# Performance work log

Hardware: AMD Instinct MI355X
Metric: run time of the kernel (lower is better)

Reference implementation:

```python
import jax, jax.numpy as jnp
import numpy as np

D_MODEL = 1024
D_STATE = 16
D_CONV = 4
D_INNER = 2 * D_MODEL  # expand=2
DT_RANK = D_MODEL // D_STATE  # ceil(1024/16) = 64


def setup_inputs() -> dict:
    key = jax.random.key(0)
    ks = jax.random.split(key, 8)
    rn = lambda k, shape, s: jax.random.normal(k, shape, jnp.float32) * s
    return {
        "x": jax.random.normal(ks[0], (4, 50, 10240), jnp.float32),
        "in_proj_w": rn(ks[1], (2 * D_INNER, D_MODEL), 0.02),
        "conv_w": rn(ks[2], (D_INNER, D_CONV), 0.2),
        "conv_b": jnp.zeros((D_INNER,), jnp.float32),
        "x_proj_w": rn(ks[3], (DT_RANK + 2 * D_STATE, D_INNER), 0.02),
        "dt_proj_w": rn(ks[4], (D_INNER, DT_RANK), 0.1),
        "dt_proj_b": jnp.log(jnp.expm1(jnp.full((D_INNER,), 0.01, jnp.float32))),
        "A_log": jnp.log(jnp.tile(jnp.arange(1, D_STATE + 1, dtype=jnp.float32), (D_INNER, 1))),
        "D": jnp.ones((D_INNER,), jnp.float32),
        "out_proj_w": rn(ks[5], (D_MODEL, D_INNER), 0.02),
        "fc1_w": rn(ks[6], (D_MODEL, 10240), 0.01),
        "fc1_b": jnp.zeros((D_MODEL,), jnp.float32),
    }


def _mamba(x, in_proj_w, conv_w, conv_b, x_proj_w, dt_proj_w, dt_proj_b, A_log, Dp, out_proj_w):
    # x: (B, L, d_model)
    B, L, _ = x.shape
    xz = x @ in_proj_w.T                          # (B, L, 2*d_inner)
    xi, z = jnp.split(xz, 2, axis=-1)             # (B, L, d_inner) each
    # causal depthwise conv1d along L
    xc = jnp.transpose(xi, (0, 2, 1))             # (B, d_inner, L)
    kern = conv_w[:, None, :]                     # (d_inner, 1, K)
    xc = jax.lax.conv_general_dilated(
        xc, kern, window_strides=(1,), padding=[(D_CONV - 1, 0)],
        dimension_numbers=("NCH", "OIH", "NCH"), feature_group_count=D_INNER)
    xc = jax.nn.silu(jnp.transpose(xc, (0, 2, 1)) + conv_b)  # (B, L, d_inner)
    # input-dependent SSM parameters
    x_dbl = xc @ x_proj_w.T                       # (B, L, dt_rank + 2*N)
    dt, Bm, Cm = jnp.split(x_dbl, [DT_RANK, DT_RANK + D_STATE], axis=-1)
    delta = jax.nn.softplus(dt @ dt_proj_w.T + dt_proj_b)    # (B, L, d_inner)
    A = -jnp.exp(A_log)                           # (d_inner, N)
    dA = jnp.exp(delta[..., None] * A)            # (B, L, d_inner, N)
    dBu = delta[..., None] * Bm[:, :, None, :] * xc[..., None]

    def step(h, ab):
        a, b = ab
        h = a * h + b
        return h, h

    h0 = jnp.zeros((B, D_INNER, D_STATE), x.dtype)
    hs = jax.lax.scan(step, h0, (jnp.swapaxes(dA, 0, 1), jnp.swapaxes(dBu, 0, 1)))[1]  # (L, B, d_inner, N)
    y = jnp.einsum("lbdn,bln->bld", hs, Cm) + xc * Dp       # (B, L, d_inner)
    y = y * jax.nn.silu(z)
    return y @ out_proj_w.T                       # (B, L, d_model)


def reference(x, in_proj_w, conv_w, conv_b, x_proj_w, dt_proj_w, dt_proj_b, A_log, D, out_proj_w, fc1_w, fc1_b):
    b, c, l = x.shape
    xm = x.reshape(b, c * 10, l // 10)            # (b, c*10, 1024)
    xm = _mamba(xm, in_proj_w, conv_w, conv_b, x_proj_w, dt_proj_w, dt_proj_b, A_log, D, out_proj_w)
    xm = xm.reshape(b, c, l)                      # (b, c, 10240)
    # dropout is identity in eval mode
    return jnp.tanh(xm @ fc1_w.T + fc1_b)         # (b, c, 1024)
```

## Files before the change

kernel.cpp:

```cpp
#include <hip/hip_runtime.h>
#include <math.h>

#define BDIM 256

constexpr int B_  = 4;
constexpr int L_  = 500;
constexpr int DM  = 1024;
constexpr int DI  = 2048;
constexpr int DXZ = 4096;
constexpr int RNK = 64;
constexpr int NST = 16;
constexpr int NXP = 96;
constexpr int M1  = B_ * L_;
constexpr int M2  = 200;
constexpr int K2  = 10240;
constexpr int NC  = 20;
constexpr int LC  = L_ / NC;

typedef __attribute__((ext_vector_type(8))) __bf16 bf16x8;
typedef __attribute__((ext_vector_type(4))) __bf16 bf16x4;
typedef __attribute__((ext_vector_type(4))) float  f32x4;

__device__ __forceinline__ float sigmoidf_(float x) { return 1.0f / (1.0f + __expf(-x)); }

template<int TR>
__device__ __forceinline__ void load_tile(const float* __restrict__ G, int ldg, int valid,
                                          float4* rg, int tid)
{
    #pragma unroll
    for (int i = 0; i < TR / 32; ++i) {
        int f = tid + i * 256;
        int r = f >> 3;
        int c = (f & 7) << 2;
        float4 v = make_float4(0.f, 0.f, 0.f, 0.f);
        if (r < valid) v = *(const float4*)(G + (size_t)r * ldg + c);
        rg[i] = v;
    }
}

template<int TR>
__device__ __forceinline__ void write_tile(const float4* rg, __bf16 (*H)[40], __bf16 (*Lo)[40], int tid)
{
    #pragma unroll
    for (int i = 0; i < TR / 32; ++i) {
        int f = tid + i * 256;
        int r = f >> 3;
        int c = (f & 7) << 2;
        float vv[4] = {rg[i].x, rg[i].y, rg[i].z, rg[i].w};
        bf16x4 hv, lv;
        #pragma unroll
        for (int j = 0; j < 4; ++j) {
            __bf16 h = (__bf16)vv[j];
            hv[j] = h;
            lv[j] = (__bf16)(vv[j] - (float)h);
        }
        *(bf16x4*)&H[r][c]  = hv;
        *(bf16x4*)&Lo[r][c] = lv;
    }
}

template<int BM, int BN, int FM, int FN, int FUSE>
__global__ __launch_bounds__(256)
void gemm_mfma(const float* __restrict__ A, int lda,
               const float* __restrict__ Bw, int ldb,
               float* __restrict__ C, int ldc,
               int M, int N, int Kchunk, long csplit_stride,
               const float* __restrict__ bias)
{
    __shared__ __bf16 Ah[BM][40], Al[BM][40], Bh[BN][40], Bl[BN][40];
    const int tid  = threadIdx.x;
    const int lane = tid & 63;
    const int wave = tid >> 6;
    const int wm = wave >> 1, wn = wave & 1;
    const int m0 = blockIdx.y * BM;
    const int n0 = blockIdx.x * BN;
    const long kbase = (long)blockIdx.z * Kchunk;
    const float* Ap = A + (size_t)m0 * lda + kbase;
    const float* Bp = Bw + (size_t)n0 * ldb + kbase;
    const int validA = min(BM, M - m0);
    const int validB = min(BN, N - n0);
    f32x4 acc[FM][FN] = {};
    const int fr = lane & 15;
    const int kq = (lane >> 4) * 8;

    float4 ra[BM / 32], rb[BN / 32];
    load_tile<BM>(Ap, lda, validA, ra, tid);
    load_tile<BN>(Bp, ldb, validB, rb, tid);

    for (int k0 = 0; k0 < Kchunk; k0 += 32) {
        write_tile<BM>(ra, Ah, Al, tid);
        write_tile<BN>(rb, Bh, Bl, tid);
        __syncthreads();
        if (k0 + 32 < Kchunk) {
            load_tile<BM>(Ap + k0 + 32, lda, validA, ra, tid);
            load_tile<BN>(Bp + k0 + 32, ldb, validB, rb, tid);
        }
        bf16x8 ah[FM], al[FM], bh[FN], bl[FN];
        #pragma unroll
        for (int i = 0; i < FM; ++i) {
            int r = wm * (FM * 16) + i * 16 + fr;
            ah[i] = *(const bf16x8*)&Ah[r][kq];
            al[i] = *(const bf16x8*)&Al[r][kq];
        }
        #pragma unroll
        for (int j = 0; j < FN; ++j) {
            int r = wn * (FN * 16) + j * 16 + fr;
            bh[j] = *(const bf16x8*)&Bh[r][kq];
            bl[j] = *(const bf16x8*)&Bl[r][kq];
        }
        #pragma unroll
        for (int i = 0; i < FM; ++i)
            #pragma unroll
            for (int j = 0; j < FN; ++j) {
                acc[i][j] = __builtin_amdgcn_mfma_f32_16x16x32_bf16(ah[i], bh[j], acc[i][j], 0, 0, 0);
                acc[i][j] = __builtin_amdgcn_mfma_f32_16x16x32_bf16(ah[i], bl[j], acc[i][j], 0, 0, 0);
                acc[i][j] = __builtin_amdgcn_mfma_f32_16x16x32_bf16(al[i], bh[j], acc[i][j], 0, 0, 0);
            }
        __syncthreads();
    }

    float* Cp = C + (size_t)blockIdx.z * csplit_stride;
    #pragma unroll
    for (int i = 0; i < FM; ++i)
        #pragma unroll
        for (int j = 0; j < FN; ++j)
            #pragma unroll
            for (int r = 0; r < 4; ++r) {
                int gm = m0 + wm * (FM * 16) + i * 16 + (lane >> 4) * 4 + r;
                int gn = n0 + wn * (FN * 16) + j * 16 + (lane & 15);
                if (gm < M && gn < N) {
                    float v = acc[i][j][r];
                    if (FUSE == 1) { v += bias[gn]; v = (v > 20.f) ? v : log1pf(__expf(v)); }
                    Cp[(size_t)gm * ldc + gn] = v;
                }
            }
}

template<int FUSE>
__global__ __launch_bounds__(256)
void reduce_k(const float* __restrict__ part, float* __restrict__ C,
              int MN, int N, int S, long stride, const float* __restrict__ bias)
{
    int i = blockIdx.x * 256 + threadIdx.x;
    if (i >= MN) return;
    float s = 0.f;
    for (int j = 0; j < S; ++j) s += part[(size_t)j * stride + i];
    if (FUSE == 2) s = tanhf(s + bias[i % N]);
    C[i] = s;
}

__global__ __launch_bounds__(BDIM)
void conv_silu_k(const float* __restrict__ xz, const float* __restrict__ cw,
                 const float* __restrict__ cb, float* __restrict__ xc)
{
    int idx = blockIdx.x * BDIM + threadIdx.x;
    if (idx >= M1 * DI) return;
    int d = idx & (DI - 1);
    int m = idx >> 11;
    int b = m / L_, l = m - b * L_;
    float acc = cb[d];
    #pragma unroll
    for (int t = 0; t < 4; ++t) {
        int ls = l - 3 + t;
        if (ls >= 0)
            acc = fmaf(cw[d * 4 + t], xz[(size_t)(b * L_ + ls) * DXZ + d], acc);
    }
    xc[idx] = acc * sigmoidf_(acc);
}


__global__ __launch_bounds__(BDIM)
void scan_partial_k(const float* __restrict__ delta, const float* __restrict__ xc,
                    const float* __restrict__ xdbl, const float* __restrict__ A_log,
                    float* __restrict__ hpart, float* __restrict__ aprod)
{
    const int t = blockIdx.x * BDIM + threadIdx.x;
    const int d = t & (DI - 1);
    const int bc = t >> 11;
    const int b = bc / NC, c = bc - b * NC;
    const int l0 = c * LC;
    float Aa[NST];
    #pragma unroll
    for (int q = 0; q < 4; ++q) {
        float4 a4 = *(const float4*)(A_log + (size_t)d * NST + q * 4);
        Aa[q*4+0] = -__expf(a4.x); Aa[q*4+1] = -__expf(a4.y);
        Aa[q*4+2] = -__expf(a4.z); Aa[q*4+3] = -__expf(a4.w);
    }
    const float* dlt = delta + ((size_t)(b * L_ + l0)) * DI + d;
    const float* xcd = xc    + ((size_t)(b * L_ + l0)) * DI + d;
    const float* bp  = xdbl  + ((size_t)(b * L_ + l0)) * NXP + RNK;
    float h[NST] = {};
    float sdv = 0.f;
    for (int l = 0; l < LC; ++l) {
        float dv = dlt[(size_t)l * DI];
        float xv = xcd[(size_t)l * DI];
        const float4* b4 = (const float4*)(bp + (size_t)l * NXP);
        float dvx = dv * xv;
        sdv += dv;
        #pragma unroll
        for (int q = 0; q < 4; ++q) {
            float4 Bq = b4[q];
            float bb[4] = {Bq.x, Bq.y, Bq.z, Bq.w};
            #pragma unroll
            for (int j = 0; j < 4; ++j) {
                int n = q * 4 + j;
                float dA = __expf(dv * Aa[n]);
                h[n] = fmaf(dA, h[n], dvx * bb[j]);
            }
        }
    }
    float4* hp4 = (float4*)(hpart + (size_t)t * NST);
    float4* ap4 = (float4*)(aprod + (size_t)t * NST);
    #pragma unroll
    for (int q = 0; q < 4; ++q) {
        hp4[q] = make_float4(h[q*4], h[q*4+1], h[q*4+2], h[q*4+3]);
        ap4[q] = make_float4(__expf(Aa[q*4+0]*sdv), __expf(Aa[q*4+1]*sdv),
                             __expf(Aa[q*4+2]*sdv), __expf(Aa[q*4+3]*sdv));
    }
}

__global__ __launch_bounds__(BDIM)
void scan_fix_k(float* __restrict__ hpart, const float* __restrict__ aprod)
{
    const int i = blockIdx.x * BDIM + threadIdx.x;
    if (i >= B_ * DI * NST) return;
    const int nn = i & (NST - 1);
    const int d  = (i >> 4) & (DI - 1);
    const int b  = i >> 15;
    float h = 0.f;
    for (int c = 0; c < NC; ++c) {
        size_t o = ((size_t)((b * NC + c) * DI + d)) * NST + nn;
        float hp = hpart[o];
        float ap = aprod[o];
        hpart[o] = h;
        h = fmaf(ap, h, hp);
    }
}

__global__ __launch_bounds__(BDIM)
void scan_final_k(const float* __restrict__ xz, const float* __restrict__ xc,
                  const float* __restrict__ xdbl, const float* __restrict__ delta,
                  const float* __restrict__ A_log, const float* __restrict__ Dp,
                  const float* __restrict__ hpre, float* __restrict__ y)
{
    const int t = blockIdx.x * BDIM + threadIdx.x;
    const int d = t & (DI - 1);
    const int bc = t >> 11;
    const int b = bc / NC, c = bc - b * NC;
    const int l0 = c * LC;
    float Aa[NST];
    #pragma unroll
    for (int q = 0; q < 4; ++q) {
        float4 a4 = *(const float4*)(A_log + (size_t)d * NST + q * 4);
        Aa[q*4+0] = -__expf(a4.x); Aa[q*4+1] = -__expf(a4.y);
        Aa[q*4+2] = -__expf(a4.z); Aa[q*4+3] = -__expf(a4.w);
    }
    float h[NST];
    const float4* h4 = (const float4*)(hpre + (size_t)t * NST);
    #pragma unroll
    for (int q = 0; q < 4; ++q) {
        float4 hv = h4[q];
        h[q*4+0] = hv.x; h[q*4+1] = hv.y; h[q*4+2] = hv.z; h[q*4+3] = hv.w;
    }
    const float Dd = Dp[d];
    const float* dlt = delta + ((size_t)(b * L_ + l0)) * DI + d;
    const float* xcd = xc    + ((size_t)(b * L_ + l0)) * DI + d;
    const float* bp  = xdbl  + ((size_t)(b * L_ + l0)) * NXP + RNK;
    const float* zp  = xz    + ((size_t)(b * L_ + l0)) * DXZ + DI + d;
    float* yp = y + ((size_t)(b * L_ + l0)) * DI + d;
    for (int l = 0; l < LC; ++l) {
        float dv = dlt[(size_t)l * DI];
        float xv = xcd[(size_t)l * DI];
        const float4* b4 = (const float4*)(bp + (size_t)l * NXP);
        float dvx = dv * xv;
        float p = 0.f;
        #pragma unroll
        for (int q = 0; q < 4; ++q) {
            float4 Bq = b4[q];
            float4 Cq = b4[4 + q];
            float bb[4] = {Bq.x, Bq.y, Bq.z, Bq.w};
            float cc[4] = {Cq.x, Cq.y, Cq.z, Cq.w};
            #pragma unroll
            for (int j = 0; j < 4; ++j) {
                int n = q * 4 + j;
                float dA = __expf(dv * Aa[n]);
                h[n] = fmaf(dA, h[n], dvx * bb[j]);
                p = fmaf(h[n], cc[j], p);
            }
        }
        float zv = zp[(size_t)l * DXZ];
        float yv = fmaf(xv, Dd, p);
        yv *= zv * sigmoidf_(zv);
        yp[(size_t)l * DI] = yv;
    }
}

extern "C" void kernel_launch(void* const* d_in, const int* in_sizes, int n_in,
                              void* d_out, int out_size, void* d_ws, size_t ws_size,
                              hipStream_t stream) {
    const float* x         = (const float*)d_in[0];
    const float* in_proj_w = (const float*)d_in[1];
    const float* conv_w    = (const float*)d_in[2];
    const float* conv_b    = (const float*)d_in[3];
    const float* x_proj_w  = (const float*)d_in[4];
    const float* dt_proj_w = (const float*)d_in[5];
    const float* dt_proj_b = (const float*)d_in[6];
    const float* A_log     = (const float*)d_in[7];
    const float* Dp        = (const float*)d_in[8];
    const float* out_proj_w= (const float*)d_in[9];
    const float* fc1_w     = (const float*)d_in[10];
    const float* fc1_b     = (const float*)d_in[11];
    float* out = (float*)d_out;

    float* ws    = (float*)d_ws;
    float* xz    = ws;
    float* xc    = xz + (size_t)M1 * DXZ;
    float* xdbl  = xc + (size_t)M1 * DI;
    float* delta = xdbl + (size_t)M1 * NXP;
    float* hpart = delta + (size_t)M1 * DI;
    float* aprod = hpart + (size_t)B_ * NC * DI * NST;
    float* y     = delta;
    float* partx = delta;
    float* partO = xz;
    float* ym    = xc;
    float* partf = delta;

    dim3 blk(BDIM);
    gemm_mfma<64,128,2,4,0><<<dim3(DXZ/128, (M1+63)/64, 1), blk, 0, stream>>>(
        x, DM, in_proj_w, DM, xz, DXZ, M1, DXZ, DM, 0, nullptr);
    conv_silu_k<<<(M1*DI + BDIM-1)/BDIM, blk, 0, stream>>>(xz, conv_w, conv_b, xc);
    gemm_mfma<64,64,2,2,0><<<dim3((NXP+63)/64, (M1+63)/64, 8), blk, 0, stream>>>(
        xc, DI, x_proj_w, DI, partx, NXP, M1, NXP, DI/8, (long)M1*NXP, nullptr);
    reduce_k<0><<<(M1*NXP + 255)/256, blk, 0, stream>>>(
        partx, xdbl, M1*NXP, NXP, 8, (long)M1*NXP, nullptr);
    gemm_mfma<64,64,2,2,1><<<dim3(DI/64, (M1+63)/64, 1), blk, 0, stream>>>(
        xdbl, NXP, dt_proj_w, RNK, delta, DI, M1, DI, RNK, 0, dt_proj_b);
    scan_partial_k<<<(B_*NC*DI)/BDIM, blk, 0, stream>>>(
        delta, xc, xdbl, A_log, hpart, aprod);
    scan_fix_k<<<(B_*DI*NST + BDIM-1)/BDIM, blk, 0, stream>>>(hpart, aprod);
    scan_final_k<<<(B_*NC*DI)/BDIM, blk, 0, stream>>>(
        xz, xc, xdbl, delta, A_log, Dp, hpart, y);
    gemm_mfma<64,64,2,2,0><<<dim3(DM/64, (M1+63)/64, 4), blk, 0, stream>>>(
        y, DI, out_proj_w, DI, partO, DM, M1, DM, DI/4, (long)M1*DM, nullptr);
    reduce_k<0><<<(M1*DM + 255)/256, blk, 0, stream>>>(
        partO, ym, M1*DM, DM, 4, (long)M1*DM, nullptr);
    gemm_mfma<64,64,2,2,0><<<dim3(DM/64, (M2+63)/64, 20), blk, 0, stream>>>(
        ym, K2, fc1_w, K2, partf, DM, M2, DM, K2/20, (long)M2*DM, nullptr);
    reduce_k<2><<<(M2*DM + 255)/256, blk, 0, stream>>>(
        partf, out, M2*DM, DM, 20, (long)M2*DM, fc1_b);
    (void)in_sizes; (void)n_in; (void)out_size; (void)ws_size;
}
```

Baseline: 288.7 us.

## Pre-split weights into bf16 hi/lo once per GEMM and enlarge in_proj tile

Adds a split kernel that converts each fp32 weight matrix into bf16 high and low halves in workspace before its GEMM. The GEMM then loads the pre-split weights directly instead of converting them per tile in every block, which removes repeated conversion work and halves the weight load width. The in_proj GEMM also moves to 128x128 tiles. The cost is extra split-kernel launches and memory passes each call, plus careful reuse of workspace regions that alias live buffers.

Measured after the change: 288.9 us. No clear change (+0.1%).

```diff
diff --git a/kernel.cpp b/kernel.cpp
--- a/kernel.cpp
+++ b/kernel.cpp
@@ -23,6 +23,25 @@
 
 __device__ __forceinline__ float sigmoidf_(float x) { return 1.0f / (1.0f + __expf(-x)); }
 
+__global__ __launch_bounds__(BDIM)
+void split_w_k(const float* __restrict__ W, __bf16* __restrict__ Wh,
+               __bf16* __restrict__ Wl, int n4)
+{
+    int i = blockIdx.x * BDIM + threadIdx.x;
+    if (i >= n4) return;
+    float4 v = *(const float4*)(W + (size_t)i * 4);
+    float vv[4] = {v.x, v.y, v.z, v.w};
+    bf16x4 hv, lv;
+    #pragma unroll
+    for (int j = 0; j < 4; ++j) {
+        __bf16 h = (__bf16)vv[j];
+        hv[j] = h;
+        lv[j] = (__bf16)(vv[j] - (float)h);
+    }
+    *(bf16x4*)(Wh + (size_t)i * 4) = hv;
+    *(bf16x4*)(Wl + (size_t)i * 4) = lv;
+}
+
 template<int TR>
 __device__ __forceinline__ void load_tile(const float* __restrict__ G, int ldg, int valid,
                                           float4* rg, int tid)
@@ -59,13 +78,46 @@
     }
 }
 
+template<int TR>
+__device__ __forceinline__ void load_wtile(const __bf16* __restrict__ Wh, const __bf16* __restrict__ Wl,
+                                           int ldb, int valid, bf16x8* rh, bf16x8* rl, int tid)
+{
+    #pragma unroll
+    for (int i = 0; i < TR / 64; ++i) {
+        int f = tid + i * 256;
+        int r = f >> 2;
+        int c = (f & 3) * 8;
+        bf16x8 hv = {}, lv = {};
+        if (r < valid) {
+            hv = *(const bf16x8*)(Wh + (size_t)r * ldb + c);
+            lv = *(const bf16x8*)(Wl + (size_t)r * ldb + c);
+        }
+        rh[i] = hv;
+        rl[i] = lv;
+    }
+}
+
+template<int TR>
+__device__ __forceinline__ void store_wtile(const bf16x8* rh, const bf16x8* rl,
+                                            __bf16 (*H)[40], __bf16 (*Lo)[40], int tid)
+{
+    #pragma unroll
+    for (int i = 0; i < TR / 64; ++i) {
+        int f = tid + i * 256;
+        int r = f >> 2;
+        int c = (f & 3) * 8;
+        *(bf16x8*)&H[r][c]  = rh[i];
+        *(bf16x8*)&Lo[r][c] = rl[i];
+    }
+}
+
 template<int BM, int BN, int FM, int FN, int FUSE>
 __global__ __launch_bounds__(256)
-void gemm_mfma(const float* __restrict__ A, int lda,
-               const float* __restrict__ Bw, int ldb,
-               float* __restrict__ C, int ldc,
-               int M, int N, int Kchunk, long csplit_stride,
-               const float* __restrict__ bias)
+void gemm_pw(const float* __restrict__ A, int lda,
+             const __bf16* __restrict__ Bwh, const __bf16* __restrict__ Bwl, int ldb,
+             float* __restrict__ C, int ldc,
+             int M, int N, int Kchunk, long csplit_stride,
+             const float* __restrict__ bias)
 {
     __shared__ __bf16 Ah[BM][40], Al[BM][40], Bh[BN][40], Bl[BN][40];
     const int tid  = threadIdx.x;
@@ -75,25 +127,27 @@
     const int m0 = blockIdx.y * BM;
     const int n0 = blockIdx.x * BN;
     const long kbase = (long)blockIdx.z * Kchunk;
-    const float* Ap = A + (size_t)m0 * lda + kbase;
-    const float* Bp = Bw + (size_t)n0 * ldb + kbase;
+    const float*  Ap  = A   + (size_t)m0 * lda + kbase;
+    const __bf16* Bph = Bwh + (size_t)n0 * ldb + kbase;
+    const __bf16* Bpl = Bwl + (size_t)n0 * ldb + kbase;
     const int validA = min(BM, M - m0);
     const int validB = min(BN, N - n0);
     f32x4 acc[FM][FN] = {};
     const int fr = lane & 15;
     const int kq = (lane >> 4) * 8;
 
-    float4 ra[BM / 32], rb[BN / 32];
+    float4 ra[BM / 32];
+    bf16x8 rbh[BN / 64], rbl[BN / 64];
     load_tile<BM>(Ap, lda, validA, ra, tid);
-    load_tile<BN>(Bp, ldb, validB, rb, tid);
+    load_wtile<BN>(Bph, Bpl, ldb, validB, rbh, rbl, tid);
 
     for (int k0 = 0; k0 < Kchunk; k0 += 32) {
         write_tile<BM>(ra, Ah, Al, tid);
-        write_tile<BN>(rb, Bh, Bl, tid);
+        store_wtile<BN>(rbh, rbl, Bh, Bl, tid);
         __syncthreads();
         if (k0 + 32 < Kchunk) {
             load_tile<BM>(Ap + k0 + 32, lda, validA, ra, tid);
-            load_tile<BN>(Bp + k0 + 32, ldb, validB, rb, tid);
+            load_wtile<BN>(Bph + k0 + 32, Bpl + k0 + 32, ldb, validB, rbh, rbl, tid);
         }
         bf16x8 ah[FM], al[FM], bh[FN], bl[FN];
         #pragma unroll
@@ -167,7 +221,6 @@
     }
     xc[idx] = acc * sigmoidf_(acc);
 }
-
 
 __global__ __launch_bounds__(BDIM)
 void scan_partial_k(const float* __restrict__ delta, const float* __restrict__ xc,
@@ -325,27 +378,43 @@
     float* ym    = xc;
     float* partf = delta;
 
+    __bf16* W1h = (__bf16*)hpart;
+    __bf16* W1l = (__bf16*)aprod;
+    __bf16* xph = (__bf16*)hpart;
+    __bf16* xpl = xph + (size_t)NXP * DI;
+    __bf16* dph = xpl + (size_t)NXP * DI;
+    __bf16* dpl = dph + (size_t)DI * RNK;
+    __bf16* W4h = (__bf16*)xc;
+    __bf16* W4l = W4h + (size_t)DM * DI;
+    __bf16* f1h = (__bf16*)xz;
+    __bf16* f1l = (__bf16*)hpart;
+
     dim3 blk(BDIM);
-    gemm_mfma<64,128,2,4,0><<<dim3(DXZ/128, (M1+63)/64, 1), blk, 0, stream>>>(
-        x, DM, in_proj_w, DM, xz, DXZ, M1, DXZ, DM, 0, nullptr);
+    split_w_k<<<(DXZ*DM/4 + 255)/256, blk, 0, stream>>>(in_proj_w, W1h, W1l, DXZ*DM/4);
+    gemm_pw<128,128,4,4,0><<<dim3(DXZ/128, (M1+127)/128, 1), blk, 0, stream>>>(
+        x, DM, W1h, W1l, DM, xz, DXZ, M1, DXZ, DM, 0, nullptr);
     conv_silu_k<<<(M1*DI + BDIM-1)/BDIM, blk, 0, stream>>>(xz, conv_w, conv_b, xc);
-    gemm_mfma<64,64,2,2,0><<<dim3((NXP+63)/64, (M1+63)/64, 8), blk, 0, stream>>>(
-        xc, DI, x_proj_w, DI, partx, NXP, M1, NXP, DI/8, (long)M1*NXP, nullptr);
+    split_w_k<<<(NXP*DI/4 + 255)/256, blk, 0, stream>>>(x_proj_w, xph, xpl, NXP*DI/4);
+    split_w_k<<<(DI*RNK/4 + 255)/256, blk, 0, stream>>>(dt_proj_w, dph, dpl, DI*RNK/4);
+    gemm_pw<64,64,2,2,0><<<dim3((NXP+63)/64, (M1+63)/64, 8), blk, 0, stream>>>(
+        xc, DI, xph, xpl, DI, partx, NXP, M1, NXP, DI/8, (long)M1*NXP, nullptr);
     reduce_k<0><<<(M1*NXP + 255)/256, blk, 0, stream>>>(
         partx, xdbl, M1*NXP, NXP, 8, (long)M1*NXP, nullptr);
-    gemm_mfma<64,64,2,2,1><<<dim3(DI/64, (M1+63)/64, 1), blk, 0, stream>>>(
-        xdbl, NXP, dt_proj_w, RNK, delta, DI, M1, DI, RNK, 0, dt_proj_b);
+    gemm_pw<64,64,2,2,1><<<dim3(DI/64, (M1+63)/64, 1), blk, 0, stream>>>(
+        xdbl, NXP, dph, dpl, RNK, delta, DI, M1, DI, RNK, 0, dt_proj_b);
     scan_partial_k<<<(B_*NC*DI)/BDIM, blk, 0, stream>>>(
         delta, xc, xdbl, A_log, hpart, aprod);
     scan_fix_k<<<(B_*DI*NST + BDIM-1)/BDIM, blk, 0, stream>>>(hpart, aprod);
     scan_final_k<<<(B_*NC*DI)/BDIM, blk, 0, stream>>>(
         xz, xc, xdbl, delta, A_log, Dp, hpart, y);
-    gemm_mfma<64,64,2,2,0><<<dim3(DM/64, (M1+63)/64, 4), blk, 0, stream>>>(
-        y, DI, out_proj_w, DI, partO, DM, M1, DM, DI/4, (long)M1*DM, nullptr);
+    split_w_k<<<(DM*DI/4 + 255)/256, blk, 0, stream>>>(out_proj_w, W4h, W4l, DM*DI/4);
+    gemm_pw<64,64,2,2,0><<<dim3(DM/64, (M1+63)/64, 4), blk, 0, stream>>>(
+        y, DI, W4h, W4l, DI, partO, DM, M1, DM, DI/4, (long)M1*DM, nullptr);
     reduce_k<0><<<(M1*DM + 255)/256, blk, 0, stream>>>(
         partO, ym, M1*DM, DM, 4, (long)M1*DM, nullptr);
-    gemm_mfma<64,64,2,2,0><<<dim3(DM/64, (M2+63)/64, 20), blk, 0, stream>>>(
-        ym, K2, fc1_w, K2, partf, DM, M2, DM, K2/20, (long)M2*DM, nullptr);
+    split_w_k<<<(DM*K2/4 + 255)/256, blk, 0, stream>>>(fc1_w, f1h, f1l, DM*K2/4);
+    gemm_pw<64,64,2,2,0><<<dim3(DM/64, (M2+63)/64, 20), blk, 0, stream>>>(
+        ym, K2, f1h, f1l, K2, partf, DM, M2, DM, K2/20, (long)M2*DM, nullptr);
     reduce_k<2><<<(M2*DM + 255)/256, blk, 0, stream>>>(
         partf, out, M2*DM, DM, 20, (long)M2*DM, fc1_b);
     (void)in_sizes; (void)n_in; (void)out_size; (void)ws_size;
```

## Pre-split weights into MFMA fragment layout and stream B from registers

Applied to the files above, without the earlier changes.

Adds a kernel that converts each weight matrix once per call into hi/lo bf16 pairs, stored in MFMA-fragment order. A new GEMM loads these B fragments straight from global memory into registers, with double buffering. This removes the per-tile fp32-to-bf16 split and LDS staging of the weights for the in_proj, x_proj, dt_proj and out_proj GEMMs, and in_proj moves to a 128x64 tile. The cost is extra conversion launches and workspace traffic on every call, plus uncoalesced-looking fragment reads that depend on cache reuse.

New measurement: 298.6 us. 1.03x slower.

```diff
diff --git a/kernel.cpp b/kernel.cpp
--- a/kernel.cpp
+++ b/kernel.cpp
@@ -23,6 +23,30 @@
 
 __device__ __forceinline__ float sigmoidf_(float x) { return 1.0f / (1.0f + __expf(-x)); }
 
+__global__ __launch_bounds__(BDIM)
+void split_w_frag_k(const float* __restrict__ W, __bf16* __restrict__ Wfh,
+                    __bf16* __restrict__ Wfl, int K, int kprs , int n8)
+{
+    int i = blockIdx.x * BDIM + threadIdx.x;
+    if (i >= n8) return;
+    int n = i >> kprs;
+    int k = (i & ((1 << kprs) - 1)) << 3;
+    const float4* s = (const float4*)(W + (size_t)n * K + k);
+    float4 v0 = s[0], v1 = s[1];
+    float vv[8] = {v0.x, v0.y, v0.z, v0.w, v1.x, v1.y, v1.z, v1.w};
+    bf16x8 hv, lv;
+    #pragma unroll
+    for (int j = 0; j < 8; ++j) {
+        __bf16 h = (__bf16)vv[j];
+        hv[j] = h;
+        lv[j] = (__bf16)(vv[j] - (float)h);
+    }
+    int lane = (n & 15) | (((k >> 3) & 3) << 4);
+    size_t idx = (((size_t)(n >> 4) * (K >> 5) + (k >> 5)) * 64 + lane) * 8;
+    *(bf16x8*)(Wfh + idx) = hv;
+    *(bf16x8*)(Wfl + idx) = lv;
+}
+
 template<int TR>
 __device__ __forceinline__ void load_tile(const float* __restrict__ G, int ldg, int valid,
                                           float4* rg, int tid)
@@ -56,6 +80,113 @@
         }
         *(bf16x4*)&H[r][c]  = hv;
         *(bf16x4*)&Lo[r][c] = lv;
+    }
+}
+
+template<int FN>
+__device__ __forceinline__ void load_bfrag(const __bf16* __restrict__ Wf,
+                                           int nbase, int N, int K, long kglob,
+                                           int lane, bf16x8* r)
+{
+    int kb = (int)(kglob >> 5);
+    #pragma unroll
+    for (int j = 0; j < FN; ++j) {
+        int n = nbase + j * 16;
+        bf16x8 v = {};
+        if (n < N) {
+            size_t idx = (((size_t)(n >> 4) * (K >> 5) + kb) * 64 + lane) * 8;
+            v = *(const bf16x8*)(Wf + idx);
+        }
+        r[j] = v;
+    }
+}
+
+template<int BM, int BN, int FM, int FN, int FUSE>
+__global__ __launch_bounds__(256)
+void gemm_frag(const float* __restrict__ A, int lda,
+               const __bf16* __restrict__ Wfh, const __bf16* __restrict__ Wfl, int K,
+               float* __restrict__ C, int ldc,
+               int M, int N, int Kchunk, long csplit_stride,
+               const float* __restrict__ bias)
+{
+    __shared__ __bf16 Ah[BM][40], Al[BM][40];
+    const int tid  = threadIdx.x;
+    const int lane = tid & 63;
+    const int wave = tid >> 6;
+    const int wm = wave >> 1, wn = wave & 1;
+    const int m0 = blockIdx.y * BM;
+    const int n0 = blockIdx.x * BN;
+    const long kbase = (long)blockIdx.z * Kchunk;
+    const float* Ap = A + (size_t)m0 * lda + kbase;
+    const int validA = min(BM, M - m0);
+    const int nbase = n0 + wn * (FN * 16);
+    f32x4 acc[FM][FN] = {};
+    const int fr = lane & 15;
+    const int kq = (lane >> 4) * 8;
+
+    float4 ra[BM / 32];
+    bf16x8 bh[FN], bl[FN], nh[FN] = {}, nl[FN] = {};
+    load_tile<BM>(Ap, lda, validA, ra, tid);
+    load_bfrag<FN>(Wfh, nbase, N, K, kbase, lane, bh);
+    load_bfrag<FN>(Wfl, nbase, N, K, kbase, lane, bl);
+
+    for (int k0 = 0; k0 < Kchunk; k0 += 32) {
+        write_tile<BM>(ra, Ah, Al, tid);
+        __syncthreads();
+        if (k0 + 32 < Kchunk) {
+            load_tile<BM>(Ap + k0 + 32, lda, validA, ra, tid);
+            load_bfrag<FN>(Wfh, nbase, N, K, kbase + k0 + 32, lane, nh);
+            load_bfrag<FN>(Wfl, nbase, N, K, kbase + k0 + 32, lane, nl);
+        }
+        bf16x8 ah[FM], al[FM];
+        #pragma unroll
+        for (int i = 0; i < FM; ++i) {
+            int r = wm * (FM * 16) + i * 16 + fr;
+            ah[i] = *(const bf16x8*)&Ah[r][kq];
+            al[i] = *(const bf16x8*)&Al[r][kq];
+        }
+        #pragma unroll
+        for (int i = 0; i < FM; ++i)
+            #pragma unroll
+            for (int j = 0; j < FN; ++j) {
+                acc[i][j] = __builtin_amdgcn_mfma_f32_16x16x32_bf16(ah[i], bh[j], acc[i][j], 0, 0, 0);
+                acc[i][j] = __builtin_amdgcn_mfma_f32_16x16x32_bf16(ah[i], bl[j], acc[i][j], 0, 0, 0);
+                acc[i][j] = __builtin_amdgcn_mfma_f32_16x16x32_bf16(al[i], bh[j], acc[i][j], 0, 0, 0);
+            }
+        __syncthreads();
+        #pragma unroll
+        for (int j = 0; j < FN; ++j) { bh[j] = nh[j]; bl[j] = nl[j]; }
+    }
+
+    float* Cp = C + (size_t)blockIdx.z * csplit_stride;
+    #pragma unroll
+    for (int i = 0; i < FM; ++i)
+        #pragma unroll
+        for (int j = 0; j < FN; ++j)
+            #pragma unroll
+            for (int r = 0; r < 4; ++r) {
+                int gm = m0 + wm * (FM * 16) + i * 16 + (lane >> 4) * 4 + r;
+                int gn = n0 + wn * (FN * 16) + j * 16 + (lane & 15);
+                if (gm < M && gn < N) {
+                    float v = acc[i][j][r];
+                    if (FUSE == 1) { v += bias[gn]; v = (v > 20.f) ? v : log1pf(__expf(v)); }
+                    Cp[(size_t)gm * ldc + gn] = v;
+                }
+            }
+}
+
+template<int TR>
+__device__ __forceinline__ void load_tile_g(const float* __restrict__ G, int ldg, int valid,
+                                            float4* rg, int tid)
+{
+    #pragma unroll
+    for (int i = 0; i < TR / 32; ++i) {
+        int f = tid + i * 256;
+        int r = f >> 3;
+        int c = (f & 7) << 2;
+        float4 v = make_float4(0.f, 0.f, 0.f, 0.f);
+        if (r < valid) v = *(const float4*)(G + (size_t)r * ldg + c);
+        rg[i] = v;
     }
 }
 
@@ -84,16 +215,16 @@
     const int kq = (lane >> 4) * 8;
 
     float4 ra[BM / 32], rb[BN / 32];
-    load_tile<BM>(Ap, lda, validA, ra, tid);
-    load_tile<BN>(Bp, ldb, validB, rb, tid);
+    load_tile_g<BM>(Ap, lda, validA, ra, tid);
+    load_tile_g<BN>(Bp, ldb, validB, rb, tid);
 
     for (int k0 = 0; k0 < Kchunk; k0 += 32) {
         write_tile<BM>(ra, Ah, Al, tid);
         write_tile<BN>(rb, Bh, Bl, tid);
         __syncthreads();
         if (k0 + 32 < Kchunk) {
-            load_tile<BM>(Ap + k0 + 32, lda, validA, ra, tid);
-            load_tile<BN>(Bp + k0 + 32, ldb, validB, rb, tid);
+            load_tile_g<BM>(Ap + k0 + 32, lda, validA, ra, tid);
+            load_tile_g<BN>(Bp + k0 + 32, ldb, validB, rb, tid);
         }
         bf16x8 ah[FM], al[FM], bh[FN], bl[FN];
         #pragma unroll
@@ -167,7 +298,6 @@
     }
     xc[idx] = acc * sigmoidf_(acc);
 }
-
 
 __global__ __launch_bounds__(BDIM)
 void scan_partial_k(const float* __restrict__ delta, const float* __restrict__ xc,
@@ -325,23 +455,36 @@
     float* ym    = xc;
     float* partf = delta;
 
+    __bf16* W1h = (__bf16*)hpart;
+    __bf16* W1l = (__bf16*)aprod;
+    __bf16* xph = (__bf16*)hpart;
+    __bf16* xpl = xph + (size_t)NXP * DI;
+    __bf16* dph = xpl + (size_t)NXP * DI;
+    __bf16* dpl = dph + (size_t)DI * RNK;
+    __bf16* W4h = (__bf16*)xc;
+    __bf16* W4l = W4h + (size_t)DM * DI;
+
     dim3 blk(BDIM);
-    gemm_mfma<64,128,2,4,0><<<dim3(DXZ/128, (M1+63)/64, 1), blk, 0, stream>>>(
-        x, DM, in_proj_w, DM, xz, DXZ, M1, DXZ, DM, 0, nullptr);
+    split_w_frag_k<<<(DXZ*DM/8 + 255)/256, blk, 0, stream>>>(in_proj_w, W1h, W1l, DM, 7, DXZ*DM/8);
+    gemm_frag<128,64,4,2,0><<<dim3(DXZ/64, (M1+127)/128, 1), blk, 0, stream>>>(
+        x, DM, W1h, W1l, DM, xz, DXZ, M1, DXZ, DM, 0, nullptr);
     conv_silu_k<<<(M1*DI + BDIM-1)/BDIM, blk, 0, stream>>>(xz, conv_w, conv_b, xc);
-    gemm_mfma<64,64,2,2,0><<<dim3((NXP+63)/64, (M1+63)/64, 8), blk, 0, stream>>>(
-        xc, DI, x_proj_w, DI, partx, NXP, M1, NXP, DI/8, (long)M1*NXP, nullptr);
+    split_w_frag_k<<<(NXP*DI/8 + 255)/256, blk, 0, stream>>>(x_proj_w, xph, xpl, DI, 8, NXP*DI/8);
+    split_w_frag_k<<<(DI*RNK/8 + 255)/256, blk, 0, stream>>>(dt_proj_w, dph, dpl, RNK, 3, DI*RNK/8);
+    gemm_frag<64,64,2,2,0><<<dim3((NXP+63)/64, (M1+63)/64, 8), blk, 0, stream>>>(
+        xc, DI, xph, xpl, DI, partx, NXP, M1, NXP, DI/8, (long)M1*NXP, nullptr);
     reduce_k<0><<<(M1*NXP + 255)/256, blk, 0, stream>>>(
         partx, xdbl, M1*NXP, NXP, 8, (long)M1*NXP, nullptr);
-    gemm_mfma<64,64,2,2,1><<<dim3(DI/64, (M1+63)/64, 1), blk, 0, stream>>>(
-        xdbl, NXP, dt_proj_w, RNK, delta, DI, M1, DI, RNK, 0, dt_proj_b);
+    gemm_frag<64,64,2,2,1><<<dim3(DI/64, (M1+63)/64, 1), blk, 0, stream>>>(
+        xdbl, NXP, dph, dpl, RNK, delta, DI, M1, DI, RNK, 0, dt_proj_b);
     scan_partial_k<<<(B_*NC*DI)/BDIM, blk, 0, stream>>>(
         delta, xc, xdbl, A_log, hpart, aprod);
     scan_fix_k<<<(B_*DI*NST + BDIM-1)/BDIM, blk, 0, stream>>>(hpart, aprod);
     scan_final_k<<<(B_*NC*DI)/BDIM, blk, 0, stream>>>(
         xz, xc, xdbl, delta, A_log, Dp, hpart, y);
-    gemm_mfma<64,64,2,2,0><<<dim3(DM/64, (M1+63)/64, 4), blk, 0, stream>>>(
-        y, DI, out_proj_w, DI, partO, DM, M1, DM, DI/4, (long)M1*DM, nullptr);
+    split_w_frag_k<<<(DM*DI/8 + 255)/256, blk, 0, stream>>>(out_proj_w, W4h, W4l, DI, 8, DM*DI/8);
+    gemm_frag<64,64,2,2,0><<<dim3(DM/64, (M1+63)/64, 4), blk, 0, stream>>>(
+        y, DI, W4h, W4l, DI, partO, DM, M1, DM, DI/4, (long)M1*DM, nullptr);
     reduce_k<0><<<(M1*DM + 255)/256, blk, 0, stream>>>(
         partO, ym, M1*DM, DM, 4, (long)M1*DM, nullptr);
     gemm_mfma<64,64,2,2,0><<<dim3(DM/64, (M2+63)/64, 20), blk, 0, stream>>>(
```
